# Kernel tuning notes

Hardware: AMD Instinct MI355X
Metric: run time of the kernel (lower is better)

Reference implementation:

```python
import jax, jax.numpy as jnp
import numpy as np

B, S, E, H = 2, 2048, 1024, 16
HD = E // H  # head_dim = 64


def setup_inputs() -> dict:
    key = jax.random.key(0)
    k1, k2, k3, k4, k5 = jax.random.split(key, 5)
    return {
        "hidden_states": jax.random.normal(k1, (B, S, E), dtype=jnp.float32),
        "w_attn": jax.random.normal(k2, (E, 3 * E), dtype=jnp.float32) * 0.02,
        "b_attn": jax.random.normal(k3, (3 * E,), dtype=jnp.float32) * 0.02,
        "w_proj": jax.random.normal(k4, (E, E), dtype=jnp.float32) * 0.02,
        "b_proj": jax.random.normal(k5, (E,), dtype=jnp.float32) * 0.02,
    }


def reference(hidden_states, w_attn, b_attn, w_proj, b_proj):
    b, s, e = hidden_states.shape
    # QKV projection (HF Conv1D: x @ W + b)
    qkv = hidden_states @ w_attn + b_attn  # [B,S,3E]
    q, k, v = jnp.split(qkv, 3, axis=-1)
    # [B,S,E] -> [B,H,S,HD]
    def split_heads(x):
        return x.reshape(b, s, H, HD).transpose(0, 2, 1, 3)
    q, k, v = split_heads(q), split_heads(k), split_heads(v)
    scale = 1.0 / float(HD) ** 0.5  # scale_attn_weights
    scores = jnp.einsum("bhqd,bhkd->bhqk", q, k) * scale  # [B,H,S,S]
    causal = jnp.tril(jnp.ones((s, s), dtype=bool))
    mask_value = jnp.finfo(scores.dtype).min
    scores = jnp.where(causal, scores, mask_value)
    attn = jax.nn.softmax(scores, axis=-1)
    # attn_dropout is identity (p=0.0)
    out = jnp.einsum("bhqk,bhkd->bhqd", attn, v)  # [B,H,S,HD]
    out = out.transpose(0, 2, 1, 3).reshape(b, s, e)  # merge heads
    out = out @ w_proj + b_proj  # c_proj; resid_dropout identity
    return out
```

## Files before the change

### kernel.cpp

```cpp
#include <hip/hip_runtime.h>
#include <hip/hip_bf16.h>

#define B_   2
#define S_   2048
#define E_   1024
#define H_   16
#define HD_  64
#define E3_  3072
#define M_   4096
#define QKS  2048
#define QSC  0.1803368801111f

using short8 = __attribute__((ext_vector_type(8))) short;
using f32x4  = __attribute__((ext_vector_type(4))) float;

__device__ __forceinline__ unsigned short f2bf(float f) {
  union { float f; unsigned v; } t; t.f = f;
  unsigned r = t.v + 0x7FFFu + ((t.v >> 16) & 1u);
  return (unsigned short)(r >> 16);
}

__device__ __forceinline__ float bf2f(unsigned short u) {
  union { unsigned v; float f; } t; t.v = ((unsigned)u) << 16; return t.f;
}

__device__ __forceinline__ float exp2_fast(float x) {
  float r;
  asm("v_exp_f32 %0, %1" : "=v"(r) : "v"(x));
  return r;
}

__device__ __forceinline__ void gload16(const void* g, void* l) {
  __builtin_amdgcn_global_load_lds(
      (const __attribute__((address_space(1))) unsigned int*)g,
      (__attribute__((address_space(3))) unsigned int*)l, 16, 0, 0);
}

__global__ __launch_bounds__(256) void prep(
    const float* __restrict__ X, const float* __restrict__ Wa,
    const float* __restrict__ Wp,
    unsigned short* __restrict__ Xb, unsigned short* __restrict__ WaT,
    unsigned short* __restrict__ WpT) {
  __shared__ float tile[32][33];
  const int id = blockIdx.x;
  if (id < 4096) {
    const int i = (id * 256 + threadIdx.x) * 4;
    float4 v = *(const float4*)(X + i);
    ushort4 o;
    o.x = f2bf(v.x); o.y = f2bf(v.y); o.z = f2bf(v.z); o.w = f2bf(v.w);
    *(ushort4*)(Xb + i) = o;
  } else {
    const float* W; unsigned short* WT; int N, bn, bk;
    if (id < 7168) {
      W = Wa; WT = WaT; N = E3_;
      const int j = id - 4096; bn = (j % 96) * 32; bk = (j / 96) * 32;
    } else {
      W = Wp; WT = WpT; N = E_;
      const int j = id - 7168; bn = (j & 31) * 32; bk = (j >> 5) * 32;
    }
    const int tx = threadIdx.x & 31, ty = threadIdx.x >> 5;
    #pragma unroll
    for (int i2 = 0; i2 < 32; i2 += 8)
      tile[ty + i2][tx] = W[(size_t)(bk + ty + i2) * N + bn + tx];
    __syncthreads();
    #pragma unroll
    for (int i2 = 0; i2 < 32; i2 += 8)
      WT[(size_t)(bn + ty + i2) * E_ + bk + tx] = f2bf(tile[tx][ty + i2]);
  }
}

template <int MODE>
__global__ __launch_bounds__(256) void gemm_bt_bias(
    const unsigned short* __restrict__ A,
    const unsigned short* __restrict__ BT,
    const float* __restrict__ bias,
    float* __restrict__ Cf,
    unsigned short* __restrict__ Cbf,
    unsigned short* __restrict__ Vt,
    int M, int N, int K) {
  __shared__ __align__(16) unsigned short As[128 * 64];
  __shared__ __align__(16) unsigned short Bs[128 * 64];
  const int t = threadIdx.x;
  const int lane = t & 63, w = t >> 6;
  const int wr = w >> 1, wc = w & 1;
  const int m0 = blockIdx.y * 128, n0 = blockIdx.x * 128;
  const int lrow = lane & 15, lkg = lane >> 4;
  const int srow = t >> 3;
  const int sc8  = (t & 7) * 8;
  const int sgc  = sc8 ^ (((t >> 3) & 7) << 3);

  f32x4 acc[4][4];
  const f32x4 z = {0.f, 0.f, 0.f, 0.f};
  #pragma unroll
  for (int i = 0; i < 4; ++i)
    #pragma unroll
    for (int j = 0; j < 4; ++j) acc[i][j] = z;

  for (int k0 = 0; k0 < K; k0 += 64) {
    __syncthreads();
    #pragma unroll
    for (int p = 0; p < 4; ++p) {
      const int r = srow + 32 * p;
      gload16(A  + (size_t)(m0 + r) * K + k0 + sgc, &As[r * 64 + sc8]);
      gload16(BT + (size_t)(n0 + r) * K + k0 + sgc, &Bs[r * 64 + sc8]);
    }
    __syncthreads();

    short8 af[4][2], bf[4][2];
    #pragma unroll
    for (int m = 0; m < 4; ++m) {
      const int row = wr * 64 + m * 16 + lrow;
      const int base = row * 64, sw = (row & 7) << 3;
      af[m][0] = *(const short8*)&As[base + ((lkg * 8) ^ sw)];
      af[m][1] = *(const short8*)&As[base + ((32 + lkg * 8) ^ sw)];
    }
    #pragma unroll
    for (int n = 0; n < 4; ++n) {
      const int row = wc * 64 + n * 16 + lrow;
      const int base = row * 64, sw = (row & 7) << 3;
      bf[n][0] = *(const short8*)&Bs[base + ((lkg * 8) ^ sw)];
      bf[n][1] = *(const short8*)&Bs[base + ((32 + lkg * 8) ^ sw)];
    }
    #pragma unroll
    for (int m = 0; m < 4; ++m)
      #pragma unroll
      for (int n = 0; n < 4; ++n) {
        acc[m][n] = __builtin_amdgcn_mfma_f32_16x16x32_bf16(af[m][0], bf[n][0],
                                                            acc[m][n], 0, 0, 0);
        acc[m][n] = __builtin_amdgcn_mfma_f32_16x16x32_bf16(af[m][1], bf[n][1],
                                                            acc[m][n], 0, 0, 0);
      }
  }

  const int r0 = (lane >> 4) * 4, c0 = lane & 15;
  #pragma unroll
  for (int m = 0; m < 4; ++m) {
    #pragma unroll
    for (int n = 0; n < 4; ++n) {
      const int row = m0 + wr * 64 + m * 16 + r0;
      const int col = n0 + wc * 64 + n * 16 + c0;
      const float bv = bias[col];
      if (MODE == 0) {
        #pragma unroll
        for (int r = 0; r < 4; ++r)
          Cf[(size_t)(row + r) * N + col] = acc[m][n][r] + bv;
      } else {
        if (col < 2 * E_) {
          const float sc = (col < E_) ? QSC : 1.0f;
          #pragma unroll
          for (int r = 0; r < 4; ++r)
            Cbf[(size_t)(row + r) * QKS + col] = f2bf((acc[m][n][r] + bv) * sc);
        } else {
          const int hd = col - 2 * E_;
          ushort4 o;
          o.x = f2bf(acc[m][n][0] + bv);
          o.y = f2bf(acc[m][n][1] + bv);
          o.z = f2bf(acc[m][n][2] + bv);
          o.w = f2bf(acc[m][n][3] + bv);
          *(ushort4*)&Vt[(((size_t)(row >> 11) * H_ + (hd >> 6)) * HD_ +
                          (hd & 63)) * (size_t)S_ + (row & 2047)] = o;
        }
      }
    }
  }
}

template __global__ void gemm_bt_bias<0>(
    const unsigned short*, const unsigned short*, const float*, float*,
    unsigned short*, unsigned short*, int, int, int);

__global__ __launch_bounds__(256) void gemm_proj(
    const unsigned short* __restrict__ A,
    const unsigned short* __restrict__ BT,
    const float* __restrict__ bias,
    float* __restrict__ Cf, int M, int N, int K) {
  __shared__ __align__(16) unsigned short As[128 * 64];
  __shared__ __align__(16) unsigned short Bs[64 * 64];
  const int t = threadIdx.x;
  const int lane = t & 63, w = t >> 6;
  const int wr = w >> 1, wc = w & 1;
  const int m0 = blockIdx.y * 128, n0 = blockIdx.x * 64;
  const int lrow = lane & 15, lkg = lane >> 4;
  const int srow = t >> 3;
  const int sc8  = (t & 7) * 8;
  const int sgc  = sc8 ^ (((t >> 3) & 7) << 3);

  f32x4 acc[4][2];
  const f32x4 z = {0.f, 0.f, 0.f, 0.f};
  #pragma unroll
  for (int i = 0; i < 4; ++i) { acc[i][0] = z; acc[i][1] = z; }

  for (int k0 = 0; k0 < K; k0 += 64) {
    __syncthreads();
    #pragma unroll
    for (int p = 0; p < 4; ++p) {
      const int r = srow + 32 * p;
      gload16(A + (size_t)(m0 + r) * K + k0 + sgc, &As[r * 64 + sc8]);
    }
    #pragma unroll
    for (int p = 0; p < 2; ++p) {
      const int r = srow + 32 * p;
      gload16(BT + (size_t)(n0 + r) * K + k0 + sgc, &Bs[r * 64 + sc8]);
    }
    __syncthreads();

    short8 af[4][2], bf[2][2];
    #pragma unroll
    for (int m = 0; m < 4; ++m) {
      const int row = wr * 64 + m * 16 + lrow;
      const int base = row * 64, sw = (row & 7) << 3;
      af[m][0] = *(const short8*)&As[base + ((lkg * 8) ^ sw)];
      af[m][1] = *(const short8*)&As[base + ((32 + lkg * 8) ^ sw)];
    }
    #pragma unroll
    for (int n = 0; n < 2; ++n) {
      const int row = wc * 32 + n * 16 + lrow;
      const int base = row * 64, sw = (row & 7) << 3;
      bf[n][0] = *(const short8*)&Bs[base + ((lkg * 8) ^ sw)];
      bf[n][1] = *(const short8*)&Bs[base + ((32 + lkg * 8) ^ sw)];
    }
    #pragma unroll
    for (int m = 0; m < 4; ++m)
      #pragma unroll
      for (int n = 0; n < 2; ++n) {
        acc[m][n] = __builtin_amdgcn_mfma_f32_16x16x32_bf16(af[m][0], bf[n][0],
                                                            acc[m][n], 0, 0, 0);
        acc[m][n] = __builtin_amdgcn_mfma_f32_16x16x32_bf16(af[m][1], bf[n][1],
                                                            acc[m][n], 0, 0, 0);
      }
  }

  const int r0 = (lane >> 4) * 4, c0 = lane & 15;
  #pragma unroll
  for (int m = 0; m < 4; ++m) {
    #pragma unroll
    for (int n = 0; n < 2; ++n) {
      const int row = m0 + wr * 64 + m * 16 + r0;
      const int col = n0 + wc * 32 + n * 16 + c0;
      const float bv = bias[col];
      #pragma unroll
      for (int r = 0; r < 4; ++r)
        Cf[(size_t)(row + r) * N + col] = acc[m][n][r] + bv;
    }
  }
}

__global__ __launch_bounds__(512) void flash_attn(
    const unsigned short* __restrict__ qk,
    const unsigned short* __restrict__ Vt,
    unsigned short* __restrict__ aout,
    unsigned short* __restrict__ Opart,
    float* __restrict__ Lpart) {
  __shared__ __align__(16) unsigned short Ks[3][64 * 64];
  __shared__ __align__(16) unsigned short Vs[3][64 * 64];

  const int t = threadIdx.x, lane = t & 63, w = t >> 6;
  const int bh = blockIdx.x;
  const int yy = blockIdx.y;
  int qt, lo, hi, part = 0;
  bool split = false;
  if (yy < 8) {
    qt = yy; lo = 0; hi = 2 * qt + 2;
  } else if (yy < 16) {
    qt = 15 - (yy - 8); part = 0; split = true;
    lo = 0; hi = qt + 1;
  } else {
    qt = 15 - (yy - 16); part = 1; split = true;
    lo = qt + 1; hi = 2 * qt + 2;
  }
  const int b = bh >> 4, h = bh & 15;
  const int lq = lane & 15;
  const int g  = lane >> 4;
  const int lk8 = g * 8;
  const int swzq = (lq & 7) << 3;
  const size_t basebs = (size_t)b * S_;
  const f32x4 z = {0.f, 0.f, 0.f, 0.f};
  const short8 ones = {(short)0x3F80, (short)0x3F80, (short)0x3F80,
                       (short)0x3F80, (short)0x3F80, (short)0x3F80,
                       (short)0x3F80, (short)0x3F80};

  short8 qf[2];
  {
    const int qrow = qt * 128 + w * 16 + lq;
    const unsigned short* qp = qk + (basebs + qrow) * QKS + h * HD_;
    qf[0] = *(const short8*)(qp + lk8);
    qf[1] = *(const short8*)(qp + 32 + lk8);
  }

  f32x4 l_acc = z;
  f32x4 o_acc[4];
  #pragma unroll
  for (int n = 0; n < 4; ++n) o_acc[n] = z;

  const int sr = t >> 3;
  const int scc = (t & 7) * 8;
  const unsigned short* kp =
      qk + (basebs + sr) * QKS + E_ + h * HD_ + (scc ^ ((sr & 7) << 3));
  const unsigned short* vp =
      Vt + ((size_t)bh * HD_ + sr) * S_ + (scc ^ ((sr & 7) << 3));

  auto stage = [&](int kt) {
    const int buf = kt % 3;
    gload16(kp + (size_t)kt * 64 * QKS, &Ks[buf][t * 8]);
    gload16(vp + (size_t)kt * 64,       &Vs[buf][t * 8]);
  };

  stage(lo);
  if (lo + 1 < hi) stage(lo + 1);

  for (int kt = lo; kt < hi; ++kt) {
    if (kt < hi - 1) {
      asm volatile("s_waitcnt vmcnt(2)" ::: "memory");
    } else {
      asm volatile("s_waitcnt vmcnt(0)" ::: "memory");
    }
    __builtin_amdgcn_sched_barrier(0);
    __builtin_amdgcn_s_barrier();
    __builtin_amdgcn_sched_barrier(0);

    if (kt + 2 < hi) stage(kt + 2);

    const int cur = kt % 3;
    const int krel = kt - 2 * qt;
    const bool skip = (krel == 1) && (w < 4);
    if (!skip) {
      f32x4 st[4];
      __builtin_amdgcn_s_setprio(1);
      #pragma unroll
      for (int f = 0; f < 4; ++f) {
        const int rowb = (f * 16 + lq) * 64;
        short8 kf0 = *(const short8*)&Ks[cur][rowb + (lk8 ^ swzq)];
        short8 kf1 = *(const short8*)&Ks[cur][rowb + ((lk8 + 32) ^ swzq)];
        st[f] = __builtin_amdgcn_mfma_f32_16x16x32_bf16(kf0, qf[0], z, 0, 0, 0);
        st[f] = __builtin_amdgcn_mfma_f32_16x16x32_bf16(kf1, qf[1], st[f], 0, 0, 0);
      }
      __builtin_amdgcn_s_setprio(0);

      if (krel >= 0) {
        const int qcol = w * 16 + lq;
        const int kbase = krel * 64;
        #pragma unroll
        for (int f = 0; f < 4; ++f)
          #pragma unroll
          for (int r = 0; r < 4; ++r)
            if (kbase + 16 * f + 4 * g + r > qcol) st[f][r] = -1e30f;
      }

      unsigned pw[4][2];
      #pragma unroll
      for (int f = 0; f < 4; ++f) {
        float p0 = exp2_fast(st[f][0]);
        float p1 = exp2_fast(st[f][1]);
        float p2 = exp2_fast(st[f][2]);
        float p3 = exp2_fast(st[f][3]);
        asm("v_cvt_pk_bf16_f32 %0, %1, %2" : "=v"(pw[f][0]) : "v"(p0), "v"(p1));
        asm("v_cvt_pk_bf16_f32 %0, %1, %2" : "=v"(pw[f][1]) : "v"(p2), "v"(p3));
      }

      unsigned c1a = pw[0][0], c1b = pw[1][0];
      unsigned c2a = pw[0][1], c2b = pw[1][1];
      unsigned c3a = pw[2][0], c3b = pw[3][0];
      unsigned c4a = pw[2][1], c4b = pw[3][1];
      asm("v_permlane32_swap_b32 %0, %1" : "+v"(c1a), "+v"(c1b));
      asm("v_permlane16_swap_b32 %0, %1" : "+v"(c1a), "+v"(c1b));
      asm("v_permlane32_swap_b32 %0, %1" : "+v"(c2a), "+v"(c2b));
      asm("v_permlane16_swap_b32 %0, %1" : "+v"(c2a), "+v"(c2b));
      asm("v_permlane32_swap_b32 %0, %1" : "+v"(c3a), "+v"(c3b));
      asm("v_permlane16_swap_b32 %0, %1" : "+v"(c3a), "+v"(c3b));
      asm("v_permlane32_swap_b32 %0, %1" : "+v"(c4a), "+v"(c4b));
      asm("v_permlane16_swap_b32 %0, %1" : "+v"(c4a), "+v"(c4b));
      union U8 { unsigned u[4]; short8 s; };
      U8 pa0u = {{c1a, c2a, c1b, c2b}};
      U8 pa1u = {{c3a, c4a, c3b, c4b}};
      const short8 pa0 = pa0u.s, pa1 = pa1u.s;

      __builtin_amdgcn_s_setprio(1);
      #pragma unroll
      for (int n = 0; n < 4; ++n) {
        const int rowb = (n * 16 + lq) * 64;
        short8 vb0 = *(const short8*)&Vs[cur][rowb + (lk8 ^ swzq)];
        short8 vb1 = *(const short8*)&Vs[cur][rowb + ((lk8 + 32) ^ swzq)];
        o_acc[n] = __builtin_amdgcn_mfma_f32_16x16x32_bf16(pa0, vb0, o_acc[n], 0, 0, 0);
        o_acc[n] = __builtin_amdgcn_mfma_f32_16x16x32_bf16(pa1, vb1, o_acc[n], 0, 0, 0);
      }
      l_acc = __builtin_amdgcn_mfma_f32_16x16x32_bf16(pa0, ones, l_acc, 0, 0, 0);
      l_acc = __builtin_amdgcn_mfma_f32_16x16x32_bf16(pa1, ones, l_acc, 0, 0, 0);
      __builtin_amdgcn_s_setprio(0);
    }
    __builtin_amdgcn_sched_barrier(0);
  }

  if (!split) {
    const int qbase = qt * 128 + w * 16 + 4 * g;
    #pragma unroll
    for (int r = 0; r < 4; ++r) {
      const float inv = 1.0f / l_acc[r];
      const int row = qbase + r;
      #pragma unroll
      for (int n = 0; n < 4; ++n)
        aout[(basebs + row) * E_ + h * HD_ + n * 16 + lq] =
            f2bf(o_acc[n][r] * inv);
    }
  } else {
    const int sidx = (bh << 3) | (qt - 8);
    unsigned short* Ob = Opart + ((size_t)(sidx * 2 + part) << 13);
    #pragma unroll
    for (int r = 0; r < 4; ++r) {
      const int qrow = w * 16 + 4 * g + r;
      #pragma unroll
      for (int n = 0; n < 4; ++n)
        Ob[qrow * 64 + n * 16 + lq] = f2bf(o_acc[n][r]);
    }
    if (lq == 0) {
      #pragma unroll
      for (int r = 0; r < 4; ++r)
        Lpart[(sidx * 2 + part) * 128 + w * 16 + 4 * g + r] = l_acc[r];
    }
  }
}

__global__ __launch_bounds__(256) void attn_combine(
    const unsigned short* __restrict__ Opart, const float* __restrict__ Lpart,
    unsigned short* __restrict__ aout) {
  const int s = blockIdx.x;
  const int bh = s >> 3, qtb = 8 + (s & 7);
  const int b = bh >> 4, h = bh & 15;
  const int t = threadIdx.x;
  const int q = t >> 1;
  const int d0 = (t & 1) * 32;
  const float l = Lpart[(s * 2 + 0) * 128 + q] + Lpart[(s * 2 + 1) * 128 + q];
  const float inv = 1.0f / l;
  const unsigned short* p0 = Opart + ((size_t)(s * 2 + 0) << 13) + q * 64 + d0;
  const unsigned short* p1 = Opart + ((size_t)(s * 2 + 1) << 13) + q * 64 + d0;
  unsigned short* dst =
      aout + ((size_t)b * S_ + qtb * 128 + q) * E_ + h * HD_ + d0;
  #pragma unroll
  for (int i = 0; i < 32; ++i)
    dst[i] = f2bf((bf2f(p0[i]) + bf2f(p1[i])) * inv);
}

extern "C" void kernel_launch(void* const* d_in, const int* in_sizes, int n_in,
                              void* d_out, int out_size, void* d_ws, size_t ws_size,
                              hipStream_t stream) {
  const float* X  = (const float*)d_in[0];
  const float* Wa = (const float*)d_in[1];
  const float* ba = (const float*)d_in[2];
  const float* Wp = (const float*)d_in[3];
  const float* bp = (const float*)d_in[4];
  float* out = (float*)d_out;

  char* ws = (char*)d_ws;
  unsigned short* Xb  = (unsigned short*)ws; ws += (size_t)M_ * E_ * 2;
  unsigned short* WaT = (unsigned short*)ws; ws += (size_t)E3_ * E_ * 2;
  unsigned short* WpT = (unsigned short*)ws; ws += (size_t)E_ * E_ * 2;
  unsigned short* QK  = (unsigned short*)ws; ws += (size_t)M_ * QKS * 2;
  unsigned short* Vt  = (unsigned short*)ws; ws += (size_t)M_ * E_ * 2;
  unsigned short* AO  = (unsigned short*)ws; ws += (size_t)M_ * E_ * 2;
  unsigned short* Opart = (unsigned short*)ws;
  ws += (size_t)256 * 2 * 128 * 64 * 2;
  float* Lpart = (float*)ws; ws += (size_t)256 * 2 * 128 * 4;

  prep<<<8192, 256, 0, stream>>>(X, Wa, Wp, Xb, WaT, WpT);
  gemm_bt_bias<1><<<dim3(E3_ / 128, M_ / 128), 256, 0, stream>>>(
      Xb, WaT, ba, nullptr, QK, Vt, M_, E3_, E_);
  flash_attn<<<dim3(B_ * H_, 24), 512, 0, stream>>>(QK, Vt, AO, Opart, Lpart);
  attn_combine<<<256, 256, 0, stream>>>(Opart, Lpart, AO);
  gemm_proj<<<dim3(E_ / 64, M_ / 128), 256, 0, stream>>>(
      AO, WpT, bp, out, M_, E_, E_);
}
```

Before: 96.73 us.

## Halve flash-attention block to 4 waves, each handling two 16-row query chunks

The attention kernel now launches 256 threads instead of 512. Each wave processes two 16-row query sub-tiles, so every K and V fragment loaded from shared memory is reused across both chunks. Each thread stages twice as many global-to-LDS loads per tile, and the vmcnt wait is raised to match. This cuts LDS read traffic per MFMA and barrier participants, at the cost of more registers per thread and fewer waves per block to hide latency.

```diff
diff --git a/kernel.cpp b/kernel.cpp
--- a/kernel.cpp
+++ b/kernel.cpp
@@ -245,7 +245,7 @@
   }
 }
 
-__global__ __launch_bounds__(512) void flash_attn(
+__global__ __launch_bounds__(256) void flash_attn(
     const unsigned short* __restrict__ qk,
     const unsigned short* __restrict__ Vt,
     unsigned short* __restrict__ aout,
@@ -279,30 +279,39 @@
                        (short)0x3F80, (short)0x3F80, (short)0x3F80,
                        (short)0x3F80, (short)0x3F80};
 
-  short8 qf[2];
-  {
-    const int qrow = qt * 128 + w * 16 + lq;
+  short8 qf[2][2];
+  #pragma unroll
+  for (int c = 0; c < 2; ++c) {
+    const int qrow = qt * 128 + c * 64 + w * 16 + lq;
     const unsigned short* qp = qk + (basebs + qrow) * QKS + h * HD_;
-    qf[0] = *(const short8*)(qp + lk8);
-    qf[1] = *(const short8*)(qp + 32 + lk8);
-  }
-
-  f32x4 l_acc = z;
-  f32x4 o_acc[4];
-  #pragma unroll
-  for (int n = 0; n < 4; ++n) o_acc[n] = z;
+    qf[c][0] = *(const short8*)(qp + lk8);
+    qf[c][1] = *(const short8*)(qp + 32 + lk8);
+  }
+
+  f32x4 l_acc[2] = {z, z};
+  f32x4 o_acc[2][4];
+  #pragma unroll
+  for (int c = 0; c < 2; ++c)
+    #pragma unroll
+    for (int n = 0; n < 4; ++n) o_acc[c][n] = z;
 
   const int sr = t >> 3;
   const int scc = (t & 7) * 8;
-  const unsigned short* kp =
+  const unsigned short* kp0 =
       qk + (basebs + sr) * QKS + E_ + h * HD_ + (scc ^ ((sr & 7) << 3));
-  const unsigned short* vp =
+  const unsigned short* kp1 = kp0 + 32 * QKS;
+  const unsigned short* vp0 =
       Vt + ((size_t)bh * HD_ + sr) * S_ + (scc ^ ((sr & 7) << 3));
+  const unsigned short* vp1 = vp0 + 32 * S_;
 
   auto stage = [&](int kt) {
     const int buf = kt % 3;
-    gload16(kp + (size_t)kt * 64 * QKS, &Ks[buf][t * 8]);
-    gload16(vp + (size_t)kt * 64,       &Vs[buf][t * 8]);
+    const size_t koff = (size_t)kt * 64 * QKS;
+    const size_t voff = (size_t)kt * 64;
+    gload16(kp0 + koff, &Ks[buf][t * 8]);
+    gload16(kp1 + koff, &Ks[buf][t * 8 + 2048]);
+    gload16(vp0 + voff, &Vs[buf][t * 8]);
+    gload16(vp1 + voff, &Vs[buf][t * 8 + 2048]);
   };
 
   stage(lo);
@@ -310,7 +319,7 @@
 
   for (int kt = lo; kt < hi; ++kt) {
     if (kt < hi - 1) {
-      asm volatile("s_waitcnt vmcnt(2)" ::: "memory");
+      asm volatile("s_waitcnt vmcnt(4)" ::: "memory");
     } else {
       asm volatile("s_waitcnt vmcnt(0)" ::: "memory");
     }
@@ -322,28 +331,35 @@
 
     const int cur = kt % 3;
     const int krel = kt - 2 * qt;
-    const bool skip = (krel == 1) && (w < 4);
-    if (!skip) {
+
+    short8 kf[4][2];
+    #pragma unroll
+    for (int f = 0; f < 4; ++f) {
+      const int rowb = (f * 16 + lq) * 64;
+      kf[f][0] = *(const short8*)&Ks[cur][rowb + (lk8 ^ swzq)];
+      kf[f][1] = *(const short8*)&Ks[cur][rowb + ((lk8 + 32) ^ swzq)];
+    }
+
+    short8 pa[2][2];
+    #pragma unroll
+    for (int c = 0; c < 2; ++c) {
+      if (krel == 1 && c == 0) continue;
       f32x4 st[4];
       __builtin_amdgcn_s_setprio(1);
       #pragma unroll
       for (int f = 0; f < 4; ++f) {
-        const int rowb = (f * 16 + lq) * 64;
-        short8 kf0 = *(const short8*)&Ks[cur][rowb + (lk8 ^ swzq)];
-        short8 kf1 = *(const short8*)&Ks[cur][rowb + ((lk8 + 32) ^ swzq)];
-        st[f] = __builtin_amdgcn_mfma_f32_16x16x32_bf16(kf0, qf[0], z, 0, 0, 0);
-        st[f] = __builtin_amdgcn_mfma_f32_16x16x32_bf16(kf1, qf[1], st[f], 0, 0, 0);
+        st[f] = __builtin_amdgcn_mfma_f32_16x16x32_bf16(kf[f][0], qf[c][0], z, 0, 0, 0);
+        st[f] = __builtin_amdgcn_mfma_f32_16x16x32_bf16(kf[f][1], qf[c][1], st[f], 0, 0, 0);
       }
       __builtin_amdgcn_s_setprio(0);
 
-      if (krel >= 0) {
+      if (krel == c) {
         const int qcol = w * 16 + lq;
-        const int kbase = krel * 64;
         #pragma unroll
         for (int f = 0; f < 4; ++f)
           #pragma unroll
           for (int r = 0; r < 4; ++r)
-            if (kbase + 16 * f + 4 * g + r > qcol) st[f][r] = -1e30f;
+            if (16 * f + 4 * g + r > qcol) st[f][r] = -1e30f;
       }
 
       unsigned pw[4][2];
@@ -372,49 +388,68 @@
       union U8 { unsigned u[4]; short8 s; };
       U8 pa0u = {{c1a, c2a, c1b, c2b}};
       U8 pa1u = {{c3a, c4a, c3b, c4b}};
-      const short8 pa0 = pa0u.s, pa1 = pa1u.s;
-
-      __builtin_amdgcn_s_setprio(1);
+      pa[c][0] = pa0u.s;
+      pa[c][1] = pa1u.s;
+    }
+
+    #pragma unroll
+    for (int f = 0; f < 4; ++f) {
+      const int rowb = (f * 16 + lq) * 64;
+      kf[f][0] = *(const short8*)&Vs[cur][rowb + (lk8 ^ swzq)];
+      kf[f][1] = *(const short8*)&Vs[cur][rowb + ((lk8 + 32) ^ swzq)];
+    }
+    __builtin_amdgcn_s_setprio(1);
+    #pragma unroll
+    for (int c = 0; c < 2; ++c) {
+      if (krel == 1 && c == 0) continue;
       #pragma unroll
       for (int n = 0; n < 4; ++n) {
-        const int rowb = (n * 16 + lq) * 64;
-        short8 vb0 = *(const short8*)&Vs[cur][rowb + (lk8 ^ swzq)];
-        short8 vb1 = *(const short8*)&Vs[cur][rowb + ((lk8 + 32) ^ swzq)];
-        o_acc[n] = __builtin_amdgcn_mfma_f32_16x16x32_bf16(pa0, vb0, o_acc[n], 0, 0, 0);
-        o_acc[n] = __builtin_amdgcn_mfma_f32_16x16x32_bf16(pa1, vb1, o_acc[n], 0, 0, 0);
-      }
-      l_acc = __builtin_amdgcn_mfma_f32_16x16x32_bf16(pa0, ones, l_acc, 0, 0, 0);
-      l_acc = __builtin_amdgcn_mfma_f32_16x16x32_bf16(pa1, ones, l_acc, 0, 0, 0);
-      __builtin_amdgcn_s_setprio(0);
-    }
+        o_acc[c][n] = __builtin_amdgcn_mfma_f32_16x16x32_bf16(pa[c][0], kf[n][0],
+                                                              o_acc[c][n], 0, 0, 0);
+        o_acc[c][n] = __builtin_amdgcn_mfma_f32_16x16x32_bf16(pa[c][1], kf[n][1],
+                                                              o_acc[c][n], 0, 0, 0);
+      }
+      l_acc[c] = __builtin_amdgcn_mfma_f32_16x16x32_bf16(pa[c][0], ones,
+                                                         l_acc[c], 0, 0, 0);
+      l_acc[c] = __builtin_amdgcn_mfma_f32_16x16x32_bf16(pa[c][1], ones,
+                                                         l_acc[c], 0, 0, 0);
+    }
+    __builtin_amdgcn_s_setprio(0);
     __builtin_amdgcn_sched_barrier(0);
   }
 
   if (!split) {
-    const int qbase = qt * 128 + w * 16 + 4 * g;
-    #pragma unroll
-    for (int r = 0; r < 4; ++r) {
-      const float inv = 1.0f / l_acc[r];
-      const int row = qbase + r;
-      #pragma unroll
-      for (int n = 0; n < 4; ++n)
-        aout[(basebs + row) * E_ + h * HD_ + n * 16 + lq] =
-            f2bf(o_acc[n][r] * inv);
+    #pragma unroll
+    for (int c = 0; c < 2; ++c) {
+      const int qbase = qt * 128 + c * 64 + w * 16 + 4 * g;
+      #pragma unroll
+      for (int r = 0; r < 4; ++r) {
+        const float inv = 1.0f / l_acc[c][r];
+        const int row = qbase + r;
+        #pragma unroll
+        for (int n = 0; n < 4; ++n)
+          aout[(basebs + row) * E_ + h * HD_ + n * 16 + lq] =
+              f2bf(o_acc[c][n][r] * inv);
+      }
     }
   } else {
     const int sidx = (bh << 3) | (qt - 8);
     unsigned short* Ob = Opart + ((size_t)(sidx * 2 + part) << 13);
     #pragma unroll
-    for (int r = 0; r < 4; ++r) {
-      const int qrow = w * 16 + 4 * g + r;
-      #pragma unroll
-      for (int n = 0; n < 4; ++n)
-        Ob[qrow * 64 + n * 16 + lq] = f2bf(o_acc[n][r]);
-    }
-    if (lq == 0) {
-      #pragma unroll
-      for (int r = 0; r < 4; ++r)
-        Lpart[(sidx * 2 + part) * 128 + w * 16 + 4 * g + r] = l_acc[r];
+    for (int c = 0; c < 2; ++c) {
+      #pragma unroll
+      for (int r = 0; r < 4; ++r) {
+        const int qrow = c * 64 + w * 16 + 4 * g + r;
+        #pragma unroll
+        for (int n = 0; n < 4; ++n)
+          Ob[qrow * 64 + n * 16 + lq] = f2bf(o_acc[c][n][r]);
+      }
+      if (lq == 0) {
+        #pragma unroll
+        for (int r = 0; r < 4; ++r)
+          Lpart[(sidx * 2 + part) * 128 + c * 64 + w * 16 + 4 * g + r] =
+              l_acc[c][r];
+      }
     }
   }
 }
@@ -463,7 +498,7 @@
   prep<<<8192, 256, 0, stream>>>(X, Wa, Wp, Xb, WaT, WpT);
   gemm_bt_bias<1><<<dim3(E3_ / 128, M_ / 128), 256, 0, stream>>>(
       Xb, WaT, ba, nullptr, QK, Vt, M_, E3_, E_);
-  flash_attn<<<dim3(B_ * H_, 24), 512, 0, stream>>>(QK, Vt, AO, Opart, Lpart);
+  flash_attn<<<dim3(B_ * H_, 24), 256, 0, stream>>>(QK, Vt, AO, Opart, Lpart);
   attn_combine<<<256, 256, 0, stream>>>(Opart, Lpart, AO);
   gemm_proj<<<dim3(E_ / 64, M_ / 128), 256, 0, stream>>>(
       AO, WpT, bp, out, M_, E_, E_);
```

New measurement: 103.2 us. 1.07x slower.
